# Kernel tuning notes

Measured on AMD Instinct MI355X. Metric: run time of the kernel, lower is better.

Reference implementation:

```python
import jax, jax.numpy as jnp
import numpy as np

N = 320          # number of valid codes in the batch
D = 128          # spatial dims; embeddings are (N, D+1) Lorentz points
MIN_DIST = 0.1
MARGIN = 0.1
WEIGHT = 0.1


def setup_inputs() -> dict:
    key = jax.random.key(0)
    k1, k2 = jax.random.split(key)
    # Valid hyperboloid points: x0 = sqrt(1 + ||x_spatial||^2)
    sp = 0.5 * jax.random.normal(k1, (N, D), dtype=jnp.float32)
    x0 = jnp.sqrt(1.0 + jnp.sum(sp * sp, axis=-1, keepdims=True))
    embeddings = jnp.concatenate([x0, sp], axis=-1)  # (N, D+1)
    # Symmetric nonnegative tree-distance matrix with zero diagonal
    td = jax.random.uniform(k2, (N, N), dtype=jnp.float32) * 8.0
    td = 0.5 * (td + td.T)
    td = td * (1.0 - jnp.eye(N, dtype=jnp.float32))
    return {"embeddings": embeddings, "tree_distances": td}


def _lorentz_pairwise(x):
    # Lorentz (hyperboloid) distance: d = arccosh(-<x,y>_L),
    # <x,y>_L = -x0*y0 + x_sp . y_sp
    t = x[:, :1]
    sp = x[:, 1:]
    inner = sp @ sp.T - t @ t.T  # (N, N) Minkowski inner product
    return jnp.arccosh(jnp.clip(-inner, 1.0 + 1e-7, None))


def reference(embeddings, tree_distances):
    emb = _lorentz_pairwise(embeddings)      # (N, N) embedding distances
    gt = tree_distances                       # (N, N) ground-truth distances
    n = gt.shape[0]
    # valid[a, j]: gt distance >= min_distance and j != a
    valid = (gt >= MIN_DIST) & (~jnp.eye(n, dtype=bool))
    # axes: (anchor a, j, k).  s > 0 iff gt[a,j] < gt[a,k]
    s = jnp.sign(gt[:, None, :] - gt[:, :, None])          # (N, N, N)
    diff = emb[:, :, None] - emb[:, None, :]                # e_j - e_k
    viol = jax.nn.relu(s * diff + MARGIN)                   # (N, N, N)
    tri = jnp.triu(jnp.ones((n, n), dtype=bool), 1)[None]   # j < k
    mask = valid[:, :, None] & valid[:, None, :] & tri & (s != 0.0)
    total = jnp.sum(jnp.where(mask, viol, 0.0))
    count = jnp.sum((viol > 0.0) & mask).astype(jnp.float32)
    return WEIGHT * jnp.where(count > 0.0, total / jnp.maximum(count, 1.0), 0.0)
```

## Files before the change

kernel.cpp:

```cpp
#include <hip/hip_runtime.h>
#include <math.h>

#define NN 320
#define DFULL 129
#define MIN_DIST_F 0.1f
#define MARGIN_F 0.1f
#define WEIGHT_F 0.1f
#define NTILE 20
#define NTRI (NTILE*(NTILE+1)/2)
#define JLEN 80
#define NCHUNK 14
#define NPART (NN*NCHUNK)

#define KG_PACK 0x0043322211110000ULL
#define JC_PACK 0x0033232132103210ULL

__device__ __forceinline__ int tri_off(int a) { return a * NTILE - (a * (a - 1)) / 2; }

__global__ __launch_bounds__(256) void lorentz_kernel(const float* __restrict__ E,
                                                      const float* __restrict__ gt,
                                                      float* __restrict__ embp) {
    const int t = blockIdx.x;
    float fa = (2.0f * NTILE + 1.0f - sqrtf((2.0f*NTILE+1.0f)*(2.0f*NTILE+1.0f) - 8.0f * (float)t)) * 0.5f;
    int a = (int)fa;
    if (a > 0 && tri_off(a) > t) --a;
    if (tri_off(a + 1) <= t) ++a;
    const int b = a + (t - tri_off(a));
    const int i0 = a * 16, j0 = b * 16;

    __shared__ float As[16][DFULL];
    __shared__ float Bs[16][DFULL];
    for (int q = threadIdx.x; q < 16 * DFULL; q += 256) {
        int r = q / DFULL, c = q - r * DFULL;
        As[r][c] = E[(i0 + r) * DFULL + c];
        Bs[r][c] = E[(j0 + r) * DFULL + c];
    }
    __syncthreads();
    const int ti = threadIdx.x & 15;
    const int tj = threadIdx.x >> 4;
    const int i = i0 + tj, j = j0 + ti;
    float tt = As[tj][0] * Bs[ti][0];
    float ss = 0.0f;
    #pragma unroll
    for (int d = 1; d < DFULL; ++d) ss = fmaf(As[tj][d], Bs[ti][d], ss);
    float x = fmaxf(tt - ss, 1.0f + 1e-7f);
    float e = acoshf(x);
    float g = gt[i * NN + j];
    float ep = (g >= MIN_DIST_F && i != j) ? e : __builtin_nanf("");
    embp[i * NN + j] = ep;
    embp[j * NN + i] = ep;
}

__global__ __launch_bounds__(64) void loss_kernel(const float* __restrict__ embp,
                                                  const float* __restrict__ gt,
                                                  float2* __restrict__ partial) {
    const int i    = blockIdx.x;
    const int y    = blockIdx.y;
    const int kg   = (int)((KG_PACK >> (4 * y)) & 0xF);
    const int jc   = (int)((JC_PACK >> (4 * y)) & 0xF);
    const int lane = threadIdx.x;
    const int k    = (kg << 6) + lane;

    const float* __restrict__ erow = embp + i * NN;
    const float* __restrict__ grow = gt   + i * NN;
    const float ek = erow[k];
    const float gk = grow[k];
    const int j0 = jc * JLEN;

    float tot = 0.0f;
    int   cnt = 0;
    #pragma unroll
    for (int jb = 0; jb < JLEN; jb += 4) {
        const float4 e4 = *reinterpret_cast<const float4*>(erow + j0 + jb);
        const float4 g4 = *reinterpret_cast<const float4*>(grow + j0 + jb);
        {   const int j = j0 + jb;
            float d = gk - g4.x; float v = fmaf(copysignf(1.0f, d), e4.x - ek, MARGIN_F);
            bool p = (v > 0.0f) && (j > k); tot += p ? v : 0.0f; cnt += (int)__popcll(__ballot(p)); }
        {   const int j = j0 + jb + 1;
            float d = gk - g4.y; float v = fmaf(copysignf(1.0f, d), e4.y - ek, MARGIN_F);
            bool p = (v > 0.0f) && (j > k); tot += p ? v : 0.0f; cnt += (int)__popcll(__ballot(p)); }
        {   const int j = j0 + jb + 2;
            float d = gk - g4.z; float v = fmaf(copysignf(1.0f, d), e4.z - ek, MARGIN_F);
            bool p = (v > 0.0f) && (j > k); tot += p ? v : 0.0f; cnt += (int)__popcll(__ballot(p)); }
        {   const int j = j0 + jb + 3;
            float d = gk - g4.w; float v = fmaf(copysignf(1.0f, d), e4.w - ek, MARGIN_F);
            bool p = (v > 0.0f) && (j > k); tot += p ? v : 0.0f; cnt += (int)__popcll(__ballot(p)); }
    }

    for (int off = 32; off > 0; off >>= 1) tot += __shfl_down(tot, off, 64);
    if (lane == 0) partial[y * NN + i] = make_float2(tot, (float)cnt);
}

__global__ __launch_bounds__(NN) void finalize_kernel(const float2* __restrict__ partial,
                                                      float* __restrict__ out) {
    const int t = threadIdx.x;
    float T = 0.0f, C = 0.0f;
    #pragma unroll
    for (int q = 0; q < NCHUNK; ++q) {
        float2 p = partial[q * NN + t];
        T += p.x; C += p.y;
    }
    for (int off = 32; off > 0; off >>= 1) {
        T += __shfl_down(T, off, 64);
        C += __shfl_down(C, off, 64);
    }
    __shared__ float wt[5], wc[5];
    const int lane = t & 63, wid = t >> 6;
    if (lane == 0) { wt[wid] = T; wc[wid] = C; }
    __syncthreads();
    if (t == 0) {
        float Tt = 0.0f, Ct = 0.0f;
        #pragma unroll
        for (int w = 0; w < 5; w++) { Tt += wt[w]; Ct += wc[w]; }
        out[0] = (Ct > 0.0f) ? WEIGHT_F * Tt / Ct : 0.0f;
    }
}

extern "C" void kernel_launch(void* const* d_in, const int* in_sizes, int n_in,
                              void* d_out, int out_size, void* d_ws, size_t ws_size,
                              hipStream_t stream) {
    const float* E  = (const float*)d_in[0];
    const float* gt = (const float*)d_in[1];
    float* out = (float*)d_out;
    float2* partial = (float2*)d_ws;
    float*  embp = (float*)((char*)d_ws + 65536);

    lorentz_kernel<<<NTRI, 256, 0, stream>>>(E, gt, embp);
    dim3 g2(NN, NCHUNK);
    loss_kernel<<<g2, 64, 0, stream>>>(embp, gt, partial);
    finalize_kernel<<<1, NN, 0, stream>>>(partial, out);
}
```

Measured before the change: 22.95 us.

## Fuse three kernels into one cooperative kernel with grid-wide syncs

Replaces the three separate launches (pairwise Lorentz distance, triplet loss, finalize) with a single cooperative kernel of 256 blocks of 1024 threads. Grid syncs separate the stages so the launch gaps between kernels go away. The distance stage now uses 55 tiles of 32x32 instead of 210 tiles of 16x16, and the loss work is spread over waves in a strided loop. In exchange it pays for two grid barriers, runs only 55 active blocks during the distance phase, and needs a large 1024-thread block that may limit occupancy.

```diff
diff --git a/kernel.cpp b/kernel.cpp
--- a/kernel.cpp
+++ b/kernel.cpp
@@ -1,118 +1,128 @@
 #include <hip/hip_runtime.h>
+#include <hip/hip_cooperative_groups.h>
 #include <math.h>
+
+namespace cg = cooperative_groups;
 
 #define NN 320
 #define DFULL 129
 #define MIN_DIST_F 0.1f
 #define MARGIN_F 0.1f
 #define WEIGHT_F 0.1f
-#define NTILE 20
-#define NTRI (NTILE*(NTILE+1)/2)
-#define JLEN 80
-#define NCHUNK 14
-#define NPART (NN*NCHUNK)
+#define NT2 10
+#define NTRI2 55
+#define GBLK 256
+#define TBLK 1024
+#define NUNIT 8320
+#define NWAVES (GBLK*(TBLK/64))
 
-#define KG_PACK 0x0043322211110000ULL
-#define JC_PACK 0x0033232132103210ULL
+__device__ __forceinline__ int tri2_off(int a) { return a * NT2 - (a * (a - 1)) / 2; }
 
-__device__ __forceinline__ int tri_off(int a) { return a * NTILE - (a * (a - 1)) / 2; }
+__global__ __launch_bounds__(TBLK) void coop_kernel(const float* __restrict__ E,
+                                                    const float* __restrict__ gt,
+                                                    float* __restrict__ embp,
+                                                    float2* __restrict__ partial,
+                                                    float* __restrict__ out) {
+    const int b = blockIdx.x;
+    const int t = threadIdx.x;
+    const int lane = t & 63, wid = t >> 6;
 
-__global__ __launch_bounds__(256) void lorentz_kernel(const float* __restrict__ E,
-                                                      const float* __restrict__ gt,
-                                                      float* __restrict__ embp) {
-    const int t = blockIdx.x;
-    float fa = (2.0f * NTILE + 1.0f - sqrtf((2.0f*NTILE+1.0f)*(2.0f*NTILE+1.0f) - 8.0f * (float)t)) * 0.5f;
-    int a = (int)fa;
-    if (a > 0 && tri_off(a) > t) --a;
-    if (tri_off(a + 1) <= t) ++a;
-    const int b = a + (t - tri_off(a));
-    const int i0 = a * 16, j0 = b * 16;
+    __shared__ float As[32][DFULL];
+    __shared__ float Bs[32][DFULL];
+    __shared__ float wt[TBLK / 64];
+    __shared__ int   wc[TBLK / 64];
 
-    __shared__ float As[16][DFULL];
-    __shared__ float Bs[16][DFULL];
-    for (int q = threadIdx.x; q < 16 * DFULL; q += 256) {
-        int r = q / DFULL, c = q - r * DFULL;
-        As[r][c] = E[(i0 + r) * DFULL + c];
-        Bs[r][c] = E[(j0 + r) * DFULL + c];
+    if (b < NTRI2) {
+        float fa = (2.0f * NT2 + 1.0f - sqrtf((2.0f*NT2+1.0f)*(2.0f*NT2+1.0f) - 8.0f * (float)b)) * 0.5f;
+        int a = (int)fa;
+        if (a > 0 && tri2_off(a) > b) --a;
+        if (tri2_off(a + 1) <= b) ++a;
+        const int bb = a + (b - tri2_off(a));
+        const int i0 = a * 32, j0 = bb * 32;
+
+        for (int q = t; q < 32 * DFULL; q += TBLK) {
+            int r = q / DFULL, c = q - r * DFULL;
+            As[r][c] = E[(i0 + r) * DFULL + c];
+            Bs[r][c] = E[(j0 + r) * DFULL + c];
+        }
+        __syncthreads();
+        const int tj = t >> 5, ti = t & 31;
+        const int i = i0 + tj, j = j0 + ti;
+        float tt = As[tj][0] * Bs[ti][0];
+        float ss = 0.0f;
+        #pragma unroll
+        for (int d = 1; d < DFULL; ++d) ss = fmaf(As[tj][d], Bs[ti][d], ss);
+        float x = fmaxf(tt - ss, 1.0f + 1e-7f);
+        float e = acoshf(x);
+        float g = gt[i * NN + j];
+        float ep = (g >= MIN_DIST_F && i != j) ? e : __builtin_nanf("");
+        embp[i * NN + j] = ep;
+        if (a != bb) embp[j * NN + i] = ep;
     }
-    __syncthreads();
-    const int ti = threadIdx.x & 15;
-    const int tj = threadIdx.x >> 4;
-    const int i = i0 + tj, j = j0 + ti;
-    float tt = As[tj][0] * Bs[ti][0];
-    float ss = 0.0f;
-    #pragma unroll
-    for (int d = 1; d < DFULL; ++d) ss = fmaf(As[tj][d], Bs[ti][d], ss);
-    float x = fmaxf(tt - ss, 1.0f + 1e-7f);
-    float e = acoshf(x);
-    float g = gt[i * NN + j];
-    float ep = (g >= MIN_DIST_F && i != j) ? e : __builtin_nanf("");
-    embp[i * NN + j] = ep;
-    embp[j * NN + i] = ep;
-}
-
-__global__ __launch_bounds__(64) void loss_kernel(const float* __restrict__ embp,
-                                                  const float* __restrict__ gt,
-                                                  float2* __restrict__ partial) {
-    const int i    = blockIdx.x;
-    const int y    = blockIdx.y;
-    const int kg   = (int)((KG_PACK >> (4 * y)) & 0xF);
-    const int jc   = (int)((JC_PACK >> (4 * y)) & 0xF);
-    const int lane = threadIdx.x;
-    const int k    = (kg << 6) + lane;
-
-    const float* __restrict__ erow = embp + i * NN;
-    const float* __restrict__ grow = gt   + i * NN;
-    const float ek = erow[k];
-    const float gk = grow[k];
-    const int j0 = jc * JLEN;
+    cg::this_grid().sync();
 
     float tot = 0.0f;
     int   cnt = 0;
-    #pragma unroll
-    for (int jb = 0; jb < JLEN; jb += 4) {
-        const float4 e4 = *reinterpret_cast<const float4*>(erow + j0 + jb);
-        const float4 g4 = *reinterpret_cast<const float4*>(grow + j0 + jb);
-        {   const int j = j0 + jb;
-            float d = gk - g4.x; float v = fmaf(copysignf(1.0f, d), e4.x - ek, MARGIN_F);
-            bool p = (v > 0.0f) && (j > k); tot += p ? v : 0.0f; cnt += (int)__popcll(__ballot(p)); }
-        {   const int j = j0 + jb + 1;
-            float d = gk - g4.y; float v = fmaf(copysignf(1.0f, d), e4.y - ek, MARGIN_F);
-            bool p = (v > 0.0f) && (j > k); tot += p ? v : 0.0f; cnt += (int)__popcll(__ballot(p)); }
-        {   const int j = j0 + jb + 2;
-            float d = gk - g4.z; float v = fmaf(copysignf(1.0f, d), e4.z - ek, MARGIN_F);
-            bool p = (v > 0.0f) && (j > k); tot += p ? v : 0.0f; cnt += (int)__popcll(__ballot(p)); }
-        {   const int j = j0 + jb + 3;
-            float d = gk - g4.w; float v = fmaf(copysignf(1.0f, d), e4.w - ek, MARGIN_F);
-            bool p = (v > 0.0f) && (j > k); tot += p ? v : 0.0f; cnt += (int)__popcll(__ballot(p)); }
+    const int w = b * (TBLK / 64) + wid;
+    for (int u = w; u < NUNIT; u += NWAVES) {
+        const int i = u / 26;
+        const int c = u - i * 26;
+        int kg, jc;
+        if      (c <  8) { kg = 0; jc = c;      }
+        else if (c < 15) { kg = 1; jc = c - 7;  }
+        else if (c < 20) { kg = 2; jc = c - 12; }
+        else if (c < 24) { kg = 3; jc = c - 16; }
+        else             { kg = 4; jc = c - 18; }
+        const int k  = (kg << 6) + lane;
+        const int j0 = jc * 40;
+        const float* __restrict__ erow = embp + i * NN;
+        const float* __restrict__ grow = gt   + i * NN;
+        const float ek = erow[k];
+        const float gk = grow[k];
+        #pragma unroll
+        for (int jb = 0; jb < 40; jb += 4) {
+            const float4 e4 = *reinterpret_cast<const float4*>(erow + j0 + jb);
+            const float4 g4 = *reinterpret_cast<const float4*>(grow + j0 + jb);
+            {   const int j = j0 + jb;
+                float d = gk - g4.x; float v = fmaf(copysignf(1.0f, d), e4.x - ek, MARGIN_F);
+                bool p = (v > 0.0f) && (j > k); tot += p ? v : 0.0f; cnt += (int)__popcll(__ballot(p)); }
+            {   const int j = j0 + jb + 1;
+                float d = gk - g4.y; float v = fmaf(copysignf(1.0f, d), e4.y - ek, MARGIN_F);
+                bool p = (v > 0.0f) && (j > k); tot += p ? v : 0.0f; cnt += (int)__popcll(__ballot(p)); }
+            {   const int j = j0 + jb + 2;
+                float d = gk - g4.z; float v = fmaf(copysignf(1.0f, d), e4.z - ek, MARGIN_F);
+                bool p = (v > 0.0f) && (j > k); tot += p ? v : 0.0f; cnt += (int)__popcll(__ballot(p)); }
+            {   const int j = j0 + jb + 3;
+                float d = gk - g4.w; float v = fmaf(copysignf(1.0f, d), e4.w - ek, MARGIN_F);
+                bool p = (v > 0.0f) && (j > k); tot += p ? v : 0.0f; cnt += (int)__popcll(__ballot(p)); }
+        }
     }
-
     for (int off = 32; off > 0; off >>= 1) tot += __shfl_down(tot, off, 64);
-    if (lane == 0) partial[y * NN + i] = make_float2(tot, (float)cnt);
-}
-
-__global__ __launch_bounds__(NN) void finalize_kernel(const float2* __restrict__ partial,
-                                                      float* __restrict__ out) {
-    const int t = threadIdx.x;
-    float T = 0.0f, C = 0.0f;
-    #pragma unroll
-    for (int q = 0; q < NCHUNK; ++q) {
-        float2 p = partial[q * NN + t];
-        T += p.x; C += p.y;
-    }
-    for (int off = 32; off > 0; off >>= 1) {
-        T += __shfl_down(T, off, 64);
-        C += __shfl_down(C, off, 64);
-    }
-    __shared__ float wt[5], wc[5];
-    const int lane = t & 63, wid = t >> 6;
-    if (lane == 0) { wt[wid] = T; wc[wid] = C; }
+    if (lane == 0) { wt[wid] = tot; wc[wid] = cnt; }
     __syncthreads();
     if (t == 0) {
-        float Tt = 0.0f, Ct = 0.0f;
+        float T = 0.0f; int C = 0;
         #pragma unroll
-        for (int w = 0; w < 5; w++) { Tt += wt[w]; Ct += wc[w]; }
-        out[0] = (Ct > 0.0f) ? WEIGHT_F * Tt / Ct : 0.0f;
+        for (int q = 0; q < TBLK / 64; ++q) { T += wt[q]; C += wc[q]; }
+        partial[b] = make_float2(T, (float)C);
+    }
+    cg::this_grid().sync();
+
+    if (b == 0) {
+        float T = 0.0f, C = 0.0f;
+        if (t < GBLK) { float2 p = partial[t]; T = p.x; C = p.y; }
+        for (int off = 32; off > 0; off >>= 1) {
+            T += __shfl_down(T, off, 64);
+            C += __shfl_down(C, off, 64);
+        }
+        if (lane == 0) { wt[wid] = T; wc[wid] = C; }
+        __syncthreads();
+        if (t == 0) {
+            float Tt = 0.0f, Ct = 0.0f;
+            #pragma unroll
+            for (int q = 0; q < TBLK / 64; ++q) { Tt += wt[q]; Ct += wc[q]; }
+            out[0] = (Ct > 0.0f) ? WEIGHT_F * Tt / Ct : 0.0f;
+        }
     }
 }
 
@@ -123,10 +133,8 @@
     const float* gt = (const float*)d_in[1];
     float* out = (float*)d_out;
     float2* partial = (float2*)d_ws;
-    float*  embp = (float*)((char*)d_ws + 65536);
+    float*  embp = (float*)((char*)d_ws + 4096);
 
-    lorentz_kernel<<<NTRI, 256, 0, stream>>>(E, gt, embp);
-    dim3 g2(NN, NCHUNK);
-    loss_kernel<<<g2, 64, 0, stream>>>(embp, gt, partial);
-    finalize_kernel<<<1, NN, 0, stream>>>(partial, out);
+    void* args[] = { (void*)&E, (void*)&gt, (void*)&embp, (void*)&partial, (void*)&out };
+    hipLaunchCooperativeKernel((void*)coop_kernel, dim3(GBLK), dim3(TBLK), args, 0, stream);
 }
```

After: 79.25 us. 245% more time.
